# Kernel optimization log

Measured on AMD Instinct MI355X. Metric: run time of the kernel, lower is better.

## Reference

```python
import jax, jax.numpy as jnp
import numpy as np

OUT_H, OUT_W = 7, 7  # output_size


def _pool_matrix(in_size: int, out_size: int) -> np.ndarray:
    """[out_size, in_size] row-stochastic matrix: row o averages input
    indices in [floor(o*in/out), ceil((o+1)*in/out)) -- same windows as
    the TF adaptive pooling slicing path."""
    o = np.arange(out_size, dtype=np.float32)
    start = (o * in_size / out_size).astype(np.int32)
    stop = np.ceil((o + 1) * in_size / out_size).astype(np.int32)
    i = np.arange(in_size)
    mask = (i[None, :] >= start[:, None]) & (i[None, :] < stop[:, None])
    size = (stop - start).astype(np.float32)
    return mask.astype(np.float32) / size[:, None]


def setup_inputs() -> dict:
    key = jax.random.key(0)
    x = jax.random.normal(key, (16, 512, 512, 64), dtype=jnp.float32)
    return {"x": x}


def reference(x) -> jnp.ndarray:
    B, H, W, C = x.shape
    wh = jnp.asarray(_pool_matrix(H, OUT_H))  # [OH, H]
    ww = jnp.asarray(_pool_matrix(W, OUT_W))  # [OW, W]
    # mean over height windows, then over width windows (matches TF order)
    y = jnp.einsum('oh,bhwc->bowc', wh, x)
    y = jnp.einsum('pw,bowc->bopc', ww, y)
    return y
```

## Files before the change

kernel.cpp:

```cpp
#include <hip/hip_runtime.h>


#define IN_HW  512
#define OUT_HW 7
#define NB     16
#define C4     16
#define RPC    2
#define NCHUNK 37
#define NPAIR  (NB * OUT_HW)
#define NPIX   (NB * OUT_HW * OUT_HW)

typedef float fx4 __attribute__((ext_vector_type(4)));

__device__ __forceinline__ int win_start(int o) { return (o * IN_HW) / OUT_HW; }
__device__ __forceinline__ int win_stop(int o)  { return ((o + 1) * IN_HW + OUT_HW - 1) / OUT_HW; }

__device__ __forceinline__ void f4add(float4& a, const float4& v) {
    a.x += v.x; a.y += v.y; a.z += v.z; a.w += v.w;
}
__device__ __forceinline__ void f4addv(float4& a, const fx4& v) {
    a.x += v.x; a.y += v.y; a.z += v.z; a.w += v.w;
}

__global__ __launch_bounds__(256, 4)
void pool_stream_kernel(const float4* __restrict__ x, float4* __restrict__ partial) {
    constexpr int KJ[32] = {0,0,0,0,0, 1,1,1,1,1, 2,2,2,2, 3,3,3,3,3,
                            4,4,4,4, 5,5,5,5,5, 6,6,6,6};
    constexpr int BJ[32] = {-1,-1,-1,-1, 9, -1,-1,-1,-1, 2, -1,-1,-1, 11,
                            -1,-1,-1,-1, 4, -1,-1,-1, 13, -1,-1,-1,-1, 6,
                            -1,-1,-1,-1};

    const int blk   = blockIdx.x;
    const int chunk = blk % NCHUNK;
    const int pair  = blk / NCHUNK;
    const int oh    = pair % OUT_HW;
    const int b     = pair / OUT_HW;

    const int r0 = win_start(oh) + chunk * RPC;

    const int tid  = threadIdx.x;
    const int base = tid >> 4;
    const int c4   = tid & 15;

    float4 acc[7];
    #pragma unroll
    for (int o = 0; o < 7; ++o) acc[o] = make_float4(0.f, 0.f, 0.f, 0.f);

    #pragma unroll 1
    for (int h = r0; h < r0 + RPC; ++h) {
        const fx4* seg = (const fx4*)(x + (size_t)(b * IN_HW + h) * (IN_HW * C4) + tid);
        #pragma unroll
        for (int j = 0; j < 32; ++j) {
            fx4 v = __builtin_nontemporal_load(&seg[256 * j]);
            const int K = KJ[j];
            const int B = BJ[j];
            if (B < 0) {
                f4addv(acc[K], v);
            } else {
                if (base <= B) f4addv(acc[K], v);
                if (base >= B) f4addv(acc[K + 1], v);
            }
        }
    }

    __shared__ float4 lds[16][7][16];
    #pragma unroll
    for (int o = 0; o < 7; ++o) lds[base][o][c4] = acc[o];
    __syncthreads();

    if (tid < 7 * C4) {
        const int ow_ = tid >> 4;
        const int c_  = tid & 15;
        float4 s = make_float4(0.f, 0.f, 0.f, 0.f);
        #pragma unroll
        for (int g = 0; g < 16; ++g) f4add(s, lds[g][ow_][c_]);
        partial[((size_t)pair * NCHUNK + chunk) * (7 * C4) + tid] = s;
    }
}

__global__ __launch_bounds__(256)
void pool_finish_kernel(const float4* __restrict__ partial, float4* __restrict__ out) {
    const int idx = blockIdx.x * 256 + threadIdx.x;
    if (idx >= NPAIR * 7 * C4) return;

    const int t    = idx % (7 * C4);
    const int pair = idx / (7 * C4);
    const int ow   = t >> 4;
    const int oh   = pair % OUT_HW;

    float4 s = make_float4(0.f, 0.f, 0.f, 0.f);
    #pragma unroll 4
    for (int k = 0; k < NCHUNK; ++k) {
        float4 v = partial[((size_t)pair * NCHUNK + k) * (7 * C4) + t];
        f4add(s, v);
    }
    const float scale = 1.0f / (float)((win_stop(oh) - win_start(oh)) *
                                       (win_stop(ow) - win_start(ow)));
    s.x *= scale; s.y *= scale; s.z *= scale; s.w *= scale;
    out[idx] = s;
}

__global__ __launch_bounds__(256)
void pool_fused_kernel(const float4* __restrict__ x, float4* __restrict__ out) {
    __shared__ float4 red[256];

    const int blk = blockIdx.x;
    const int ow = blk % OUT_HW;
    const int oh = (blk / OUT_HW) % OUT_HW;
    const int b  = blk / (OUT_HW * OUT_HW);

    const int tid = threadIdx.x;
    const int c4 = tid & 15;
    const int rg = tid >> 4;

    const int hs = win_start(oh), he = win_stop(oh);
    const int ws = win_start(ow), we = win_stop(ow);

    float4 acc = make_float4(0.f, 0.f, 0.f, 0.f);
    for (int h = hs + rg; h < he; h += 16) {
        const float4* row = x + ((size_t)(b * IN_HW + h)) * (IN_HW * C4);
        #pragma unroll 8
        for (int w = ws; w < we; ++w) {
            float4 v = row[w * C4 + c4];
            f4add(acc, v);
        }
    }
    red[tid] = acc;
    __syncthreads();

    #pragma unroll
    for (int s = 8; s >= 1; s >>= 1) {
        if (rg < s) {
            float4 o = red[(rg + s) * 16 + c4];
            f4add(o, red[rg * 16 + c4]);
            red[rg * 16 + c4] = o;
        }
        __syncthreads();
    }

    if (rg == 0) {
        const float scale = 1.0f / (float)((he - hs) * (we - ws));
        float4 m = red[c4];
        m.x *= scale; m.y *= scale; m.z *= scale; m.w *= scale;
        out[(size_t)blk * C4 + c4] = m;
    }
}

extern "C" void kernel_launch(void* const* d_in, const int* in_sizes, int n_in,
                              void* d_out, int out_size, void* d_ws, size_t ws_size,
                              hipStream_t stream) {
    const float4* x = (const float4*)d_in[0];
    float4* out = (float4*)d_out;

    const size_t ws_needed = (size_t)NPAIR * NCHUNK * 7 * C4 * sizeof(float4);

    if (ws_size >= ws_needed) {
        float4* partial = (float4*)d_ws;
        pool_stream_kernel<<<NPAIR * NCHUNK, 256, 0, stream>>>(x, partial);
        pool_finish_kernel<<<(NPAIR * 7 * C4 + 255) / 256, 256, 0, stream>>>(partial, out);
    } else {
        pool_fused_kernel<<<NPIX, 256, 0, stream>>>(x, out);
    }
}
```

Before: 185.1 us.

## Replace partial-sum workspace and finish pass with per-row atomic accumulation

The two-stage scheme (per-chunk partials to workspace, then a finish kernel) is replaced by a zero-fill kernel followed by one streaming kernel. Each block reduces two input rows and atomically adds scaled sums directly into the output, into both output rows when an input row lies in overlapping windows. This drops the workspace write and read and the finish pass, and reorganises the grid to 16x256 blocks indexed by row pair. In exchange it adds many float atomics on a small output, with possible contention and nondeterministic summation order. It also hardcodes a uniform 74x74 window scale, which holds only for 512->7.

```diff
diff --git a/kernel.cpp b/kernel.cpp
--- a/kernel.cpp
+++ b/kernel.cpp
@@ -5,15 +5,9 @@
 #define OUT_HW 7
 #define NB     16
 #define C4     16
-#define RPC    2
-#define NCHUNK 37
-#define NPAIR  (NB * OUT_HW)
 #define NPIX   (NB * OUT_HW * OUT_HW)
 
 typedef float fx4 __attribute__((ext_vector_type(4)));
-
-__device__ __forceinline__ int win_start(int o) { return (o * IN_HW) / OUT_HW; }
-__device__ __forceinline__ int win_stop(int o)  { return ((o + 1) * IN_HW + OUT_HW - 1) / OUT_HW; }
 
 __device__ __forceinline__ void f4add(float4& a, const float4& v) {
     a.x += v.x; a.y += v.y; a.z += v.z; a.w += v.w;
@@ -22,33 +16,40 @@
     a.x += v.x; a.y += v.y; a.z += v.z; a.w += v.w;
 }
 
+__global__ __launch_bounds__(256)
+void pool_zero_kernel(float4* __restrict__ out) {
+    const int idx = blockIdx.x * 256 + threadIdx.x;
+    if (idx < NPIX * C4) out[idx] = make_float4(0.f, 0.f, 0.f, 0.f);
+}
+
 __global__ __launch_bounds__(256, 4)
-void pool_stream_kernel(const float4* __restrict__ x, float4* __restrict__ partial) {
+void pool_stream_atomic_kernel(const float4* __restrict__ x, float* __restrict__ out) {
     constexpr int KJ[32] = {0,0,0,0,0, 1,1,1,1,1, 2,2,2,2, 3,3,3,3,3,
                             4,4,4,4, 5,5,5,5,5, 6,6,6,6};
     constexpr int BJ[32] = {-1,-1,-1,-1, 9, -1,-1,-1,-1, 2, -1,-1,-1, 11,
                             -1,-1,-1,-1, 4, -1,-1,-1, 13, -1,-1,-1,-1, 6,
                             -1,-1,-1,-1};
+    constexpr float SCALE = 1.0f / (74.0f * 74.0f);
 
-    const int blk   = blockIdx.x;
-    const int chunk = blk % NCHUNK;
-    const int pair  = blk / NCHUNK;
-    const int oh    = pair % OUT_HW;
-    const int b     = pair / OUT_HW;
-
-    const int r0 = win_start(oh) + chunk * RPC;
+    const int blk = blockIdx.x;
+    const int rp  = blk & 255;
+    const int b   = blk >> 8;
 
     const int tid  = threadIdx.x;
     const int base = tid >> 4;
     const int c4   = tid & 15;
 
-    float4 acc[7];
+    __shared__ float4 lds[16][7][16];
+
     #pragma unroll
-    for (int o = 0; o < 7; ++o) acc[o] = make_float4(0.f, 0.f, 0.f, 0.f);
+    for (int rr = 0; rr < 2; ++rr) {
+        const int r = rp * 2 + rr;
 
-    #pragma unroll 1
-    for (int h = r0; h < r0 + RPC; ++h) {
-        const fx4* seg = (const fx4*)(x + (size_t)(b * IN_HW + h) * (IN_HW * C4) + tid);
+        float4 acc[7];
+        #pragma unroll
+        for (int o = 0; o < 7; ++o) acc[o] = make_float4(0.f, 0.f, 0.f, 0.f);
+
+        const fx4* seg = (const fx4*)(x + (size_t)(b * IN_HW + r) * (IN_HW * C4) + tid);
         #pragma unroll
         for (int j = 0; j < 32; ++j) {
             fx4 v = __builtin_nontemporal_load(&seg[256 * j]);
@@ -61,88 +62,30 @@
                 if (base >= B) f4addv(acc[K + 1], v);
             }
         }
-    }
 
-    __shared__ float4 lds[16][7][16];
-    #pragma unroll
-    for (int o = 0; o < 7; ++o) lds[base][o][c4] = acc[o];
-    __syncthreads();
+        #pragma unroll
+        for (int o = 0; o < 7; ++o) lds[base][o][c4] = acc[o];
+        __syncthreads();
 
-    if (tid < 7 * C4) {
-        const int ow_ = tid >> 4;
-        const int c_  = tid & 15;
-        float4 s = make_float4(0.f, 0.f, 0.f, 0.f);
-        #pragma unroll
-        for (int g = 0; g < 16; ++g) f4add(s, lds[g][ow_][c_]);
-        partial[((size_t)pair * NCHUNK + chunk) * (7 * C4) + tid] = s;
-    }
-}
+        if (tid < 7 * C4) {
+            const int ow_ = tid >> 4;
+            const int c_  = tid & 15;
+            float4 s = make_float4(0.f, 0.f, 0.f, 0.f);
+            #pragma unroll
+            for (int g = 0; g < 16; ++g) f4add(s, lds[g][ow_][c_]);
+            s.x *= SCALE; s.y *= SCALE; s.z *= SCALE; s.w *= SCALE;
 
-__global__ __launch_bounds__(256)
-void pool_finish_kernel(const float4* __restrict__ partial, float4* __restrict__ out) {
-    const int idx = blockIdx.x * 256 + threadIdx.x;
-    if (idx >= NPAIR * 7 * C4) return;
-
-    const int t    = idx % (7 * C4);
-    const int pair = idx / (7 * C4);
-    const int ow   = t >> 4;
-    const int oh   = pair % OUT_HW;
-
-    float4 s = make_float4(0.f, 0.f, 0.f, 0.f);
-    #pragma unroll 4
-    for (int k = 0; k < NCHUNK; ++k) {
-        float4 v = partial[((size_t)pair * NCHUNK + k) * (7 * C4) + t];
-        f4add(s, v);
-    }
-    const float scale = 1.0f / (float)((win_stop(oh) - win_start(oh)) *
-                                       (win_stop(ow) - win_start(ow)));
-    s.x *= scale; s.y *= scale; s.z *= scale; s.w *= scale;
-    out[idx] = s;
-}
-
-__global__ __launch_bounds__(256)
-void pool_fused_kernel(const float4* __restrict__ x, float4* __restrict__ out) {
-    __shared__ float4 red[256];
-
-    const int blk = blockIdx.x;
-    const int ow = blk % OUT_HW;
-    const int oh = (blk / OUT_HW) % OUT_HW;
-    const int b  = blk / (OUT_HW * OUT_HW);
-
-    const int tid = threadIdx.x;
-    const int c4 = tid & 15;
-    const int rg = tid >> 4;
-
-    const int hs = win_start(oh), he = win_stop(oh);
-    const int ws = win_start(ow), we = win_stop(ow);
-
-    float4 acc = make_float4(0.f, 0.f, 0.f, 0.f);
-    for (int h = hs + rg; h < he; h += 16) {
-        const float4* row = x + ((size_t)(b * IN_HW + h)) * (IN_HW * C4);
-        #pragma unroll 8
-        for (int w = ws; w < we; ++w) {
-            float4 v = row[w * C4 + c4];
-            f4add(acc, v);
-        }
-    }
-    red[tid] = acc;
-    __syncthreads();
-
-    #pragma unroll
-    for (int s = 8; s >= 1; s >>= 1) {
-        if (rg < s) {
-            float4 o = red[(rg + s) * 16 + c4];
-            f4add(o, red[rg * 16 + c4]);
-            red[rg * 16 + c4] = o;
+            const int oh_lo = (7 * r) >> 9;
+            const int oh_hi = (7 * r + 6) >> 9;
+            for (int oh = oh_lo; oh <= oh_hi; ++oh) {
+                float* dst = out + ((((size_t)b * OUT_HW + oh) * OUT_HW + ow_) * C4 + c_) * 4;
+                unsafeAtomicAdd(dst + 0, s.x);
+                unsafeAtomicAdd(dst + 1, s.y);
+                unsafeAtomicAdd(dst + 2, s.z);
+                unsafeAtomicAdd(dst + 3, s.w);
+            }
         }
         __syncthreads();
-    }
-
-    if (rg == 0) {
-        const float scale = 1.0f / (float)((he - hs) * (we - ws));
-        float4 m = red[c4];
-        m.x *= scale; m.y *= scale; m.z *= scale; m.w *= scale;
-        out[(size_t)blk * C4 + c4] = m;
     }
 }
 
@@ -150,15 +93,7 @@
                               void* d_out, int out_size, void* d_ws, size_t ws_size,
                               hipStream_t stream) {
     const float4* x = (const float4*)d_in[0];
-    float4* out = (float4*)d_out;
 
-    const size_t ws_needed = (size_t)NPAIR * NCHUNK * 7 * C4 * sizeof(float4);
-
-    if (ws_size >= ws_needed) {
-        float4* partial = (float4*)d_ws;
-        pool_stream_kernel<<<NPAIR * NCHUNK, 256, 0, stream>>>(x, partial);
-        pool_finish_kernel<<<(NPAIR * 7 * C4 + 255) / 256, 256, 0, stream>>>(partial, out);
-    } else {
-        pool_fused_kernel<<<NPIX, 256, 0, stream>>>(x, out);
-    }
+    pool_zero_kernel<<<(NPIX * C4 + 255) / 256, 256, 0, stream>>>((float4*)d_out);
+    pool_stream_atomic_kernel<<<NB * 256, 256, 0, stream>>>(x, (float*)d_out);
 }
```

Result: faster. 180.3 us (-2.6%).
